# Kernel optimization log

Hardware: AMD Instinct MI355X
Metric: run time of the kernel (lower is better)

The kernel has to match this reference:

```python
import jax, jax.numpy as jnp
import numpy as np

V = 32000   # vocab_size
L = 4       # n_layer
H = 12      # n_head
C = 768     # n_embd
T = 1024    # block_size / seq len
B = 4       # batch
D = C // H  # head_dim
F = 4 * C   # mlp hidden


def setup_inputs() -> dict:
    key = jax.random.key(0)
    ks = jax.random.split(key, 12)
    n = lambda k, sh: (jax.random.normal(k, sh, dtype=jnp.float32) * 0.02)
    return {
        "idx": jax.random.randint(ks[0], (B, T), 0, V, dtype=jnp.int32),
        "tok_emb": n(ks[1], (V, C)),
        "pos_emb": n(ks[2], (T, C)),
        "Wq": n(ks[3], (L, C, C)),
        "Wk": n(ks[4], (L, C, C)),
        "Wv": n(ks[5], (L, C, C)),
        "Wp": n(ks[6], (L, C, C)),
        "bp": jnp.zeros((L, C), jnp.float32),
        "ln1s": jnp.ones((L, C), jnp.float32),
        "ln1b": jnp.zeros((L, C), jnp.float32),
        "ln2s": jnp.ones((L, C), jnp.float32),
        "ln2b": jnp.zeros((L, C), jnp.float32),
        "W1": n(ks[7], (L, C, F)),
        "b1": jnp.zeros((L, F), jnp.float32),
        "W2": n(ks[8], (L, F, C)),
        "b2": jnp.zeros((L, C), jnp.float32),
        "lnfs": jnp.ones((C,), jnp.float32),
        "lnfb": jnp.zeros((C,), jnp.float32),
        "Whead": n(ks[9], (C, V)),
    }


def _ln(x, s, b):
    m = x.mean(-1, keepdims=True)
    v = ((x - m) ** 2).mean(-1, keepdims=True)
    return (x - m) * jax.lax.rsqrt(v + 1e-5) * s + b


def reference(idx, tok_emb, pos_emb, Wq, Wk, Wv, Wp, bp, ln1s, ln1b, ln2s, ln2b,
              W1, b1, W2, b2, lnfs, lnfb, Whead):
    Bc, Tc = idx.shape
    x = tok_emb[idx] + pos_emb[None, :Tc]               # [B,T,C]
    mask = jnp.tril(jnp.ones((Tc, Tc), bool))           # causal mask
    scale = 1.0 / np.sqrt(D)
    for l in range(L):
        # --- causal self-attention (explicit QK^T, masked softmax) ---
        h = _ln(x, ln1s[l], ln1b[l])
        q = (h @ Wq[l]).reshape(Bc, Tc, H, D).transpose(0, 2, 1, 3)  # [B,H,T,D]
        k = (h @ Wk[l]).reshape(Bc, Tc, H, D).transpose(0, 2, 1, 3)
        v = (h @ Wv[l]).reshape(Bc, Tc, H, D).transpose(0, 2, 1, 3)
        att = jnp.einsum('bhqd,bhkd->bhqk', q, k) * scale            # [B,H,T,T]
        att = jnp.where(mask, att, -jnp.inf)
        att = jax.nn.softmax(att, axis=-1)
        y = jnp.einsum('bhqk,bhkd->bhqd', att, v)
        y = y.transpose(0, 2, 1, 3).reshape(Bc, Tc, C)
        x = x + (y @ Wp[l] + bp[l])
        # --- GELU MLP ---
        h = _ln(x, ln2s[l], ln2b[l])
        x = x + (jax.nn.gelu(h @ W1[l] + b1[l], approximate=False) @ W2[l] + b2[l])
    x = _ln(x, lnfs, lnfb)
    logits = x @ Whead                                  # [B,T,V]
    return logits
```

## Files before the change

kernel.cpp:

```cpp
#include <hip/hip_runtime.h>
#include <stdint.h>

#define B_ 4
#define T_ 1024
#define C_ 768
#define H_ 12
#define D_ 64
#define F_ 3072
#define V_ 32000
#define L_ 4

typedef unsigned short ushort_t;
typedef __bf16 bf16x8 __attribute__((ext_vector_type(8)));
typedef float f32x4 __attribute__((ext_vector_type(4)));
typedef unsigned short u16x8 __attribute__((ext_vector_type(8)));

__device__ __forceinline__ float b2f(unsigned short u) {
    union { unsigned int i; float f; } x; x.i = ((unsigned int)u) << 16; return x.f;
}
__device__ __forceinline__ unsigned short f2b(float f) {
    union { float f; unsigned int i; } x; x.f = f;
    unsigned int r = x.i + 0x7FFFu + ((x.i >> 16) & 1u);
    return (unsigned short)(r >> 16);
}

__device__ __forceinline__ float gelu_f(float u) {
    float z = fabsf(u) * 0.70710678118654752f;
    float t = __builtin_amdgcn_rcpf(1.0f + 0.3275911f * z);
    float poly = t * (0.254829592f + t * (-0.284496736f + t * (1.421413741f +
                 t * (-1.453152027f + t * 1.061405429f))));
    float erfz = 1.0f - poly * __expf(-z * z);
    return u * 0.5f * (1.0f + copysignf(erfz, u));
}

__device__ __forceinline__ void gload16(const ushort_t* g, ushort_t* l) {
    __builtin_amdgcn_global_load_lds(
        (const __attribute__((address_space(1))) unsigned int*)g,
        (__attribute__((address_space(3))) unsigned int*)l, 16, 0, 0);
}

__global__ __launch_bounds__(256) void k_embed(const int* __restrict__ idx,
        const float* __restrict__ tok, const float* __restrict__ pos,
        float* __restrict__ x) {
    int i = blockIdx.x * 256 + threadIdx.x;
    int m = i / (C_ / 4);
    int cc = (i % (C_ / 4)) * 4;
    int t = m & (T_ - 1);
    int tokid = idx[m];
    float4 te = *(const float4*)&tok[(size_t)tokid * C_ + cc];
    float4 pe = *(const float4*)&pos[(size_t)t * C_ + cc];
    *(float4*)&x[(size_t)m * C_ + cc] =
        make_float4(te.x + pe.x, te.y + pe.y, te.z + pe.z, te.w + pe.w);
}

__global__ __launch_bounds__(256) void k_ln(const float* __restrict__ x,
        const float* __restrict__ s, const float* __restrict__ b,
        ushort_t* __restrict__ out) {
    const int lane = threadIdx.x & 63, wave = threadIdx.x >> 6;
    const int row = blockIdx.x * 4 + wave;
    const float* xr = x + (size_t)row * C_;
    float4 v[3];
    float sum = 0.f, sq = 0.f;
#pragma unroll
    for (int j = 0; j < 3; ++j) {
        v[j] = *(const float4*)&xr[lane * 4 + j * 256];
        sum += v[j].x + v[j].y + v[j].z + v[j].w;
        sq  += v[j].x * v[j].x + v[j].y * v[j].y + v[j].z * v[j].z + v[j].w * v[j].w;
    }
#pragma unroll
    for (int off = 1; off < 64; off <<= 1) {
        sum += __shfl_xor(sum, off);
        sq  += __shfl_xor(sq,  off);
    }
    float mean = sum * (1.f / C_);
    float var  = sq * (1.f / C_) - mean * mean;
    float rstd = rsqrtf(var + 1e-5f);
#pragma unroll
    for (int j = 0; j < 3; ++j) {
        int c = lane * 4 + j * 256;
        float4 sv = *(const float4*)&s[c];
        float4 bv = *(const float4*)&b[c];
        ushort4 o;
        o.x = f2b((v[j].x - mean) * rstd * sv.x + bv.x);
        o.y = f2b((v[j].y - mean) * rstd * sv.y + bv.y);
        o.z = f2b((v[j].z - mean) * rstd * sv.z + bv.z);
        o.w = f2b((v[j].w - mean) * rstd * sv.w + bv.w);
        *(ushort4*)&out[(size_t)row * C_ + c] = o;
    }
}

__global__ void k_tcvt(const float* __restrict__ in, ushort_t* __restrict__ out,
                       int R, int C) {
    __shared__ float tile[32][33];
    const float* src = in + (size_t)blockIdx.z * R * C;
    ushort_t* dst = out + (size_t)blockIdx.z * R * C;
    int r0 = blockIdx.y * 32, c0 = blockIdx.x * 32;
    int tx = threadIdx.x, ty = threadIdx.y;
#pragma unroll
    for (int i = ty; i < 32; i += 8)
        tile[i][tx] = src[(size_t)(r0 + i) * C + c0 + tx];
    __syncthreads();
#pragma unroll
    for (int i = ty; i < 32; i += 8)
        dst[(size_t)(c0 + i) * R + r0 + tx] = f2b(tile[tx][i]);
}

__global__ void k_tcvt16(const float* __restrict__ wq, const float* __restrict__ wk,
                         const float* __restrict__ wv, const float* __restrict__ wp,
                         ushort_t* __restrict__ out) {
    __shared__ float tile[32][33];
    int l = blockIdx.z >> 2, w = blockIdx.z & 3;
    const float* src = (w == 0 ? wq : w == 1 ? wk : w == 2 ? wv : wp) + (size_t)l * C_ * C_;
    ushort_t* dst = out + (size_t)blockIdx.z * C_ * C_;
    int r0 = blockIdx.y * 32, c0 = blockIdx.x * 32;
    int tx = threadIdx.x, ty = threadIdx.y;
#pragma unroll
    for (int i = ty; i < 32; i += 8)
        tile[i][tx] = src[(size_t)(r0 + i) * C_ + c0 + tx];
    __syncthreads();
#pragma unroll
    for (int i = ty; i < 32; i += 8)
        dst[(size_t)(c0 + i) * C_ + r0 + tx] = f2b(tile[tx][i]);
}

template <int EPI>
__global__ __launch_bounds__(256) void k_gemm(
        const ushort_t* __restrict__ A, const ushort_t* __restrict__ BT,
        const float* __restrict__ bias, const float* __restrict__ resid,
        float* __restrict__ outf, ushort_t* __restrict__ outb,
        ushort_t* __restrict__ outb2, ushort_t* __restrict__ outb3,
        int M, int N, int K) {
    __shared__ __align__(16) ushort_t S[24576];
    const int tid = threadIdx.x;
    const int lane = tid & 63, wave = tid >> 6;
    const int lr = lane & 15, lg = lane >> 4;
    const int wm = (wave >> 1) * 64, wn = (wave & 1) * 64;

    const int bid = blockIdx.x;
    const int m_in = bid & 7;
    const int strip = (bid >> 3) & 3;
    const int ncol = bid >> 5;
    const int m0 = (strip * 8 + m_in) << 7;
    const int n0 = ncol << 7;

    const int sr = wave * 16 + (lane >> 2);
    const int sc = (((lane & 3) ^ ((lane >> 3) & 3)) << 3);

    f32x4 acc[4][4];
#pragma unroll
    for (int i = 0; i < 4; ++i)
#pragma unroll
        for (int j = 0; j < 4; ++j) acc[i][j] = (f32x4){0.f, 0.f, 0.f, 0.f};

    auto stage = [&](int k0, int buf) {
        ushort_t* as = S + buf * 4096;
        ushort_t* bs = S + 12288 + buf * 4096;
        gload16(&A [(size_t)(m0 + sr)      * K + k0 + sc], as + (wave * 16) * 32);
        gload16(&A [(size_t)(m0 + 64 + sr) * K + k0 + sc], as + (64 + wave * 16) * 32);
        gload16(&BT[(size_t)(n0 + sr)      * K + k0 + sc], bs + (wave * 16) * 32);
        gload16(&BT[(size_t)(n0 + 64 + sr) * K + k0 + sc], bs + (64 + wave * 16) * 32);
    };

    const int nt = K >> 5;
    stage(0, 0);
    stage(32, 1);
    int cur = 0, pre = 2;
    const int swzr = (lr >> 1) & 3;
    for (int t = 0; t < nt; ++t) {
        if (t + 1 < nt) asm volatile("s_waitcnt vmcnt(4)" ::: "memory");
        else            asm volatile("s_waitcnt vmcnt(0)" ::: "memory");
        __builtin_amdgcn_sched_barrier(0);
        __builtin_amdgcn_s_barrier();
        const ushort_t* as = S + cur * 4096;
        const ushort_t* bs = S + 12288 + cur * 4096;
        bf16x8 af[4], bfr[4];
#pragma unroll
        for (int i = 0; i < 4; ++i)
            af[i]  = *(const bf16x8*)&as[(wm + i * 16 + lr) * 32 + ((lg ^ swzr) << 3)];
#pragma unroll
        for (int j = 0; j < 4; ++j)
            bfr[j] = *(const bf16x8*)&bs[(wn + j * 16 + lr) * 32 + ((lg ^ swzr) << 3)];
        if (t + 2 < nt) stage((t + 2) << 5, pre);
#pragma unroll
        for (int i = 0; i < 4; ++i)
#pragma unroll
            for (int j = 0; j < 4; ++j)
                acc[i][j] = __builtin_amdgcn_mfma_f32_16x16x32_bf16(af[i], bfr[j], acc[i][j], 0, 0, 0);
        cur = (cur == 2) ? 0 : cur + 1;
        pre = (pre == 2) ? 0 : pre + 1;
    }

    if (EPI == 2) {
        float* cls = (float*)S;
#pragma unroll
        for (int h = 0; h < 2; ++h) {
            __syncthreads();
            if ((wm >> 6) == h) {
#pragma unroll
                for (int i = 0; i < 4; ++i)
#pragma unroll
                    for (int j = 0; j < 4; ++j)
#pragma unroll
                        for (int r = 0; r < 4; ++r)
                            cls[(i * 16 + lg * 4 + r) * 128 + wn + j * 16 + lr] = acc[i][j][r];
            }
            __syncthreads();
#pragma unroll
            for (int p = 0; p < 8; ++p) {
                int row = p * 8 + (tid >> 5);
                int colc = (tid & 31) * 4;
                f32x4 val = *(const f32x4*)&cls[row * 128 + colc];
                size_t gidx = (size_t)(m0 + h * 64 + row) * N + n0 + colc;
                f32x4 rv = *(const f32x4*)&resid[gidx];
                f32x4 bv = *(const f32x4*)&bias[n0 + colc];
                val = val + rv + bv;
                *(f32x4*)&outf[gidx] = val;
            }
        }
        return;
    }

    if (EPI == 1) {
        ushort_t* cls = S;
        __syncthreads();
#pragma unroll
        for (int i = 0; i < 4; ++i)
#pragma unroll
            for (int j = 0; j < 4; ++j) {
                float bval = bias[n0 + wn + j * 16 + lr];
#pragma unroll
                for (int r = 0; r < 4; ++r)
                    cls[(wm + i * 16 + lg * 4 + r) * 128 + wn + j * 16 + lr] =
                        f2b(gelu_f(acc[i][j][r] + bval));
            }
        __syncthreads();
#pragma unroll
        for (int p = 0; p < 8; ++p) {
            int row = p * 16 + (tid >> 4);
            int colc = (tid & 15) * 8;
            u16x8 val = *(const u16x8*)&cls[row * 128 + colc];
            *(u16x8*)&outb[(size_t)(m0 + row) * N + n0 + colc] = val;
        }
        return;
    }

#pragma unroll
    for (int i = 0; i < 4; ++i) {
#pragma unroll
        for (int j = 0; j < 4; ++j) {
            int col = n0 + wn + j * 16 + lr;
#pragma unroll
            for (int r = 0; r < 4; ++r) {
                int row = m0 + wm + i * 16 + lg * 4 + r;
                float v = acc[i][j][r];
                int nm = col / 768, c = col % 768;
                int hh = c >> 6, d = c & 63;
                int bb = row >> 10, t = row & 1023;
                ushort_t val = f2b(v);
                if (nm == 0)
                    outb [((((size_t)bb * H_ + hh) << 10) + t) * D_ + d] = val;
                else if (nm == 1)
                    outb2[((((size_t)bb * H_ + hh) << 10) + t) * D_ + d] = val;
                else
                    outb3[(((size_t)bb * H_ + hh) * D_ + d) * T_ + t] = val;
            }
        }
    }
}

__global__ __launch_bounds__(512, 2) void k_gemm256b(
        const ushort_t* __restrict__ A, const ushort_t* __restrict__ BT,
        float* __restrict__ outf, int M, int N, int K) {
    __shared__ __align__(16) ushort_t S[65536];
    const int tid = threadIdx.x;
    const int lane = tid & 63, wave = tid >> 6;
    const int lr = lane & 15, lg = lane >> 4;
    const int wm = (wave >> 2) * 128, wn = (wave & 3) * 64;

    const int bid = blockIdx.x;
    const int m_in = bid & 7;
    const int strip = (bid >> 3) & 1;
    const int ncol = bid >> 4;
    const int m0 = (strip * 8 + m_in) << 8;
    const int n0 = ncol << 8;

    const int srr = lane >> 2;
    const int sc = (((lane & 3) ^ ((lane >> 3) & 3)) << 3);

    f32x4 acc[8][4];
#pragma unroll
    for (int i = 0; i < 8; ++i)
#pragma unroll
        for (int j = 0; j < 4; ++j) acc[i][j] = (f32x4){0.f, 0.f, 0.f, 0.f};

    auto stage = [&](int k0, int buf) {
        ushort_t* as = S + buf * 8192;
        ushort_t* bs = S + 32768 + buf * 8192;
#pragma unroll
        for (int q = 0; q < 2; ++q) {
            int rb = wave * 16 + q * 128;
            gload16(&A [(size_t)(m0 + rb + srr) * K + k0 + sc], as + rb * 32);
            gload16(&BT[(size_t)(n0 + rb + srr) * K + k0 + sc], bs + rb * 32);
        }
    };

    const int nt = K >> 5;
    stage(0, 0);
    stage(32, 1);
    stage(64, 2);
    const int swzr = (lr >> 1) & 3;
    for (int t = 0; t < nt; ++t) {
        int rem = nt - 1 - t;
        if (rem >= 2)      asm volatile("s_waitcnt vmcnt(8)" ::: "memory");
        else if (rem == 1) asm volatile("s_waitcnt vmcnt(4)" ::: "memory");
        else               asm volatile("s_waitcnt vmcnt(0)" ::: "memory");
        __builtin_amdgcn_sched_barrier(0);
        __builtin_amdgcn_s_barrier();
        const ushort_t* as = S + (t & 3) * 8192;
        const ushort_t* bs = S + 32768 + (t & 3) * 8192;
        if (t + 3 < nt) stage((t + 3) << 5, (t + 3) & 3);
        bf16x8 bfr[4];
#pragma unroll
        for (int j = 0; j < 4; ++j)
            bfr[j] = *(const bf16x8*)&bs[(wn + j * 16 + lr) * 32 + ((lg ^ swzr) << 3)];
#pragma unroll
        for (int i = 0; i < 8; ++i) {
            bf16x8 af = *(const bf16x8*)&as[(wm + i * 16 + lr) * 32 + ((lg ^ swzr) << 3)];
#pragma unroll
            for (int j = 0; j < 4; ++j)
                acc[i][j] = __builtin_amdgcn_mfma_f32_16x16x32_bf16(af, bfr[j], acc[i][j], 0, 0, 0);
        }
    }

    float* cls = (float*)S;
#pragma unroll
    for (int h = 0; h < 4; ++h) {
        __syncthreads();
        if ((wm >> 7) == (h >> 1)) {
            const int ibase = (h & 1) * 4;
#pragma unroll
            for (int i2 = 0; i2 < 4; ++i2)
#pragma unroll
                for (int j = 0; j < 4; ++j)
#pragma unroll
                    for (int r = 0; r < 4; ++r)
                        cls[(i2 * 16 + lg * 4 + r) * 260 + wn + j * 16 + lr] =
                            acc[ibase + i2][j][r];
        }
        __syncthreads();
#pragma unroll
        for (int p = 0; p < 8; ++p) {
            int idx = p * 512 + tid;
            int row = idx >> 6;
            int colc = (idx & 63) * 4;
            f32x4 val = *(const f32x4*)&cls[row * 260 + colc];
            __builtin_nontemporal_store(val,
                (f32x4*)&outf[(size_t)(m0 + h * 64 + row) * N + n0 + colc]);
        }
    }
}

__global__ __launch_bounds__(256) void k_attn(const ushort_t* __restrict__ q,
        const ushort_t* __restrict__ k, const ushort_t* __restrict__ vT,
        ushort_t* __restrict__ yc) {
    __shared__ __align__(16) ushort_t P[4][16 * 136];
    const int lane = threadIdx.x & 63, wave = threadIdx.x >> 6;
    const int lr = lane & 15, lg = lane >> 4;
    const int bh = blockIdx.x;
    const int bb = bh / H_, hh = bh % H_;
    const int qrow0 = (gridDim.y - 1 - blockIdx.y) * 64 + wave * 16;
    const ushort_t* qb = q + (size_t)bh * T_ * D_;
    const ushort_t* kb = k + (size_t)bh * T_ * D_;
    const ushort_t* vb = vT + (size_t)bh * D_ * T_;

    bf16x8 aq0 = *(const bf16x8*)&qb[(qrow0 + lr) * D_ + lg * 8];
    bf16x8 aq1 = *(const bf16x8*)&qb[(qrow0 + lr) * D_ + 32 + lg * 8];

    f32x4 accY[4];
    float ls = 0.f;
#pragma unroll
    for (int d = 0; d < 4; ++d) accY[d] = (f32x4){0.f, 0.f, 0.f, 0.f};

    ushort_t* pw = &P[wave][0];
    const int kv_end = qrow0 + 16;
    for (int kv0 = 0; kv0 < kv_end; kv0 += 128) {
        const bool full = (kv0 + 127 <= qrow0);
        float p[8][4];
        float ps = 0.f;
#pragma unroll
        for (int j = 0; j < 8; ++j) {
            f32x4 s = (f32x4){0.f, 0.f, 0.f, 0.f};
            bf16x8 bk0 = *(const bf16x8*)&kb[(kv0 + j * 16 + lr) * D_ + lg * 8];
            bf16x8 bk1 = *(const bf16x8*)&kb[(kv0 + j * 16 + lr) * D_ + 32 + lg * 8];
            __builtin_amdgcn_s_setprio(1);
            s = __builtin_amdgcn_mfma_f32_16x16x32_bf16(bk0, aq0, s, 0, 0, 0);
            s = __builtin_amdgcn_mfma_f32_16x16x32_bf16(bk1, aq1, s, 0, 0, 0);
            __builtin_amdgcn_s_setprio(0);
            if (full) {
#pragma unroll
                for (int r = 0; r < 4; ++r) { p[j][r] = __expf(s[r] * 0.125f); ps += p[j][r]; }
            } else {
                int kcb = kv0 + j * 16 + lg * 4;
#pragma unroll
                for (int r = 0; r < 4; ++r) {
                    p[j][r] = (kcb + r <= qrow0 + lr) ? __expf(s[r] * 0.125f) : 0.f;
                    ps += p[j][r];
                }
            }
        }
        ps += __shfl_xor(ps, 16);
        ps += __shfl_xor(ps, 32);
        ls += ps;

        asm volatile("s_waitcnt lgkmcnt(0)" ::: "memory");
        __builtin_amdgcn_sched_barrier(0);
#pragma unroll
        for (int j = 0; j < 8; ++j) {
            unsigned int w0, w1;
            asm("v_cvt_pk_bf16_f32 %0, %1, %2" : "=v"(w0) : "v"(p[j][0]), "v"(p[j][1]));
            asm("v_cvt_pk_bf16_f32 %0, %1, %2" : "=v"(w1) : "v"(p[j][2]), "v"(p[j][3]));
            uint2 w; w.x = w0; w.y = w1;
            *(uint2*)&pw[lr * 136 + j * 16 + lg * 4] = w;
        }
        asm volatile("s_waitcnt lgkmcnt(0)" ::: "memory");
        __builtin_amdgcn_sched_barrier(0);
        bf16x8 pa[4];
#pragma unroll
        for (int ks = 0; ks < 4; ++ks)
            pa[ks] = *(const bf16x8*)&pw[lr * 136 + ks * 32 + lg * 8];
#pragma unroll
        for (int d = 0; d < 4; ++d) {
            __builtin_amdgcn_s_setprio(1);
#pragma unroll
            for (int ks = 0; ks < 4; ++ks) {
                bf16x8 bv = *(const bf16x8*)&vb[(d * 16 + lr) * T_ + kv0 + ks * 32 + lg * 8];
                accY[d] = __builtin_amdgcn_mfma_f32_16x16x32_bf16(pa[ks], bv, accY[d], 0, 0, 0);
            }
            __builtin_amdgcn_s_setprio(0);
        }
    }
    float inv[4];
#pragma unroll
    for (int r = 0; r < 4; ++r) inv[r] = 1.0f / __shfl(ls, lg * 4 + r);
#pragma unroll
    for (int d = 0; d < 4; ++d)
#pragma unroll
        for (int r = 0; r < 4; ++r) {
            int row = qrow0 + lg * 4 + r;
            yc[((size_t)bb * T_ + row) * C_ + hh * D_ + d * 16 + lr] = f2b(accY[d][r] * inv[r]);
        }
}

extern "C" void kernel_launch(void* const* d_in, const int* in_sizes, int n_in,
                              void* d_out, int out_size, void* d_ws, size_t ws_size,
                              hipStream_t stream) {
    (void)in_sizes; (void)n_in; (void)out_size; (void)ws_size;
    const int*   idx  = (const int*)d_in[0];
    const float* tok  = (const float*)d_in[1];
    const float* pos  = (const float*)d_in[2];
    const float* Wq   = (const float*)d_in[3];
    const float* Wk   = (const float*)d_in[4];
    const float* Wv   = (const float*)d_in[5];
    const float* Wp   = (const float*)d_in[6];
    const float* bp   = (const float*)d_in[7];
    const float* ln1s = (const float*)d_in[8];
    const float* ln1b = (const float*)d_in[9];
    const float* ln2s = (const float*)d_in[10];
    const float* ln2b = (const float*)d_in[11];
    const float* W1   = (const float*)d_in[12];
    const float* b1   = (const float*)d_in[13];
    const float* W2   = (const float*)d_in[14];
    const float* b2   = (const float*)d_in[15];
    const float* lnfs = (const float*)d_in[16];
    const float* lnfb = (const float*)d_in[17];
    const float* Wh   = (const float*)d_in[18];
    float* out = (float*)d_out;

    char* ws = (char*)d_ws;
    size_t off = 0;
    auto alloc = [&](size_t bytes) { void* p = ws + off; off += (bytes + 255) & ~(size_t)255; return p; };

    const size_t CCE = (size_t)C_ * C_;
    const size_t CFE = (size_t)C_ * F_;
    ushort_t* wCC  = (ushort_t*)alloc(16 * CCE * 2);
    ushort_t* w1T  = (ushort_t*)alloc((size_t)L_ * CFE * 2);
    ushort_t* w2T  = (ushort_t*)alloc((size_t)L_ * CFE * 2);
    ushort_t* whT  = (ushort_t*)alloc((size_t)C_ * V_ * 2);
    float*    x    = (float*)   alloc((size_t)B_ * T_ * C_ * 4);
    ushort_t* h    = (ushort_t*)alloc((size_t)B_ * T_ * C_ * 2);
    ushort_t* qb_  = (ushort_t*)alloc((size_t)B_ * T_ * C_ * 2);
    ushort_t* kb_  = (ushort_t*)alloc((size_t)B_ * T_ * C_ * 2);
    ushort_t* vTb  = (ushort_t*)alloc((size_t)B_ * T_ * C_ * 2);
    ushort_t* yc   = (ushort_t*)alloc((size_t)B_ * T_ * C_ * 2);
    ushort_t* mh   = (ushort_t*)alloc((size_t)B_ * T_ * F_ * 2);

    dim3 tb(32, 8);
    k_tcvt16<<<dim3(24, 24, 16), tb, 0, stream>>>(Wq, Wk, Wv, Wp, wCC);
    k_tcvt<<<dim3(96, 24, 4), tb, 0, stream>>>(W1, w1T, C_, F_);
    k_tcvt<<<dim3(24, 96, 4), tb, 0, stream>>>(W2, w2T, F_, C_);
    k_tcvt<<<dim3(1000, 24, 1), tb, 0, stream>>>(Wh, whT, C_, V_);

    k_embed<<<3072, 256, 0, stream>>>(idx, tok, pos, x);

    for (int l = 0; l < L_; ++l) {
        k_ln<<<1024, 256, 0, stream>>>(x, ln1s + l * C_, ln1b + l * C_, h);
        k_gemm<3><<<18 * 32, 256, 0, stream>>>(h, wCC + (size_t)(l * 4) * CCE,
            nullptr, nullptr, nullptr, qb_, kb_, vTb, 4096, 3 * C_, C_);
        k_attn<<<dim3(48, 16), 256, 0, stream>>>(qb_, kb_, vTb, yc);
        k_gemm<2><<<6 * 32, 256, 0, stream>>>(yc, wCC + (size_t)(l * 4 + 3) * CCE,
            bp + l * C_, x, x, nullptr, nullptr, nullptr, 4096, C_, C_);
        k_ln<<<1024, 256, 0, stream>>>(x, ln2s + l * C_, ln2b + l * C_, h);
        k_gemm<1><<<24 * 32, 256, 0, stream>>>(h, w1T + (size_t)l * CFE,
            b1 + l * F_, nullptr, nullptr, mh, nullptr, nullptr, 4096, F_, C_);
        k_gemm<2><<<6 * 32, 256, 0, stream>>>(mh, w2T + (size_t)l * CFE,
            b2 + l * C_, x, x, nullptr, nullptr, nullptr, 4096, C_, F_);
    }
    k_ln<<<1024, 256, 0, stream>>>(x, lnfs, lnfb, h);
    k_gemm256b<<<2000, 512, 0, stream>>>(h, whT, out, 4096, V_, C_);
}
```

Baseline: 1.096 ms.

## Split-K the MLP down-projection and use 128-tile GEMM for LM head

The W2 GEMM (K=3072, only 192 tiles) is split into two K-halves running as 384 blocks that write fp32 partials into the reused q buffer, followed by a reduction kernel that adds bias, residual and both partials. The LM head replaces the 256x256 512-thread kernel with the generic 128x128 kernel using a new plain-store epilogue. The goal is better CU occupancy on the under-filled GEMM. The cost is extra partial-buffer traffic and a launch, and the smaller LM-head tiles give less data reuse.

```diff
diff --git a/kernel.cpp b/kernel.cpp
--- a/kernel.cpp
+++ b/kernel.cpp
@@ -190,7 +190,7 @@
         pre = (pre == 2) ? 0 : pre + 1;
     }
 
-    if (EPI == 2) {
+    if (EPI == 0 || EPI == 2) {
         float* cls = (float*)S;
 #pragma unroll
         for (int h = 0; h < 2; ++h) {
@@ -211,10 +211,14 @@
                 int colc = (tid & 31) * 4;
                 f32x4 val = *(const f32x4*)&cls[row * 128 + colc];
                 size_t gidx = (size_t)(m0 + h * 64 + row) * N + n0 + colc;
-                f32x4 rv = *(const f32x4*)&resid[gidx];
-                f32x4 bv = *(const f32x4*)&bias[n0 + colc];
-                val = val + rv + bv;
-                *(f32x4*)&outf[gidx] = val;
+                if (EPI == 2) {
+                    f32x4 rv = *(const f32x4*)&resid[gidx];
+                    f32x4 bv = *(const f32x4*)&bias[n0 + colc];
+                    val = val + rv + bv;
+                    *(f32x4*)&outf[gidx] = val;
+                } else {
+                    __builtin_nontemporal_store(val, (f32x4*)&outf[gidx]);
+                }
             }
         }
         return;
@@ -268,96 +272,106 @@
     }
 }
 
-__global__ __launch_bounds__(512, 2) void k_gemm256b(
+__global__ __launch_bounds__(256) void k_gemm_split(
         const ushort_t* __restrict__ A, const ushort_t* __restrict__ BT,
-        float* __restrict__ outf, int M, int N, int K) {
-    __shared__ __align__(16) ushort_t S[65536];
+        float* __restrict__ part, int M, int N, int Kfull, int Klen) {
+    __shared__ __align__(16) ushort_t S[24576];
     const int tid = threadIdx.x;
     const int lane = tid & 63, wave = tid >> 6;
     const int lr = lane & 15, lg = lane >> 4;
-    const int wm = (wave >> 2) * 128, wn = (wave & 3) * 64;
+    const int wm = (wave >> 1) * 64, wn = (wave & 1) * 64;
 
     const int bid = blockIdx.x;
     const int m_in = bid & 7;
-    const int strip = (bid >> 3) & 1;
-    const int ncol = bid >> 4;
-    const int m0 = (strip * 8 + m_in) << 8;
-    const int n0 = ncol << 8;
-
-    const int srr = lane >> 2;
+    const int strip = (bid >> 3) & 3;
+    const int ncol = bid >> 5;
+    const int m0 = (strip * 8 + m_in) << 7;
+    const int n0 = ncol << 7;
+    const int kb = blockIdx.y * Klen;
+    float* outf = part + (size_t)blockIdx.y * M * N;
+
+    const int sr = wave * 16 + (lane >> 2);
     const int sc = (((lane & 3) ^ ((lane >> 3) & 3)) << 3);
 
-    f32x4 acc[8][4];
-#pragma unroll
-    for (int i = 0; i < 8; ++i)
+    f32x4 acc[4][4];
+#pragma unroll
+    for (int i = 0; i < 4; ++i)
 #pragma unroll
         for (int j = 0; j < 4; ++j) acc[i][j] = (f32x4){0.f, 0.f, 0.f, 0.f};
 
     auto stage = [&](int k0, int buf) {
-        ushort_t* as = S + buf * 8192;
-        ushort_t* bs = S + 32768 + buf * 8192;
-#pragma unroll
-        for (int q = 0; q < 2; ++q) {
-            int rb = wave * 16 + q * 128;
-            gload16(&A [(size_t)(m0 + rb + srr) * K + k0 + sc], as + rb * 32);
-            gload16(&BT[(size_t)(n0 + rb + srr) * K + k0 + sc], bs + rb * 32);
-        }
+        ushort_t* as = S + buf * 4096;
+        ushort_t* bs = S + 12288 + buf * 4096;
+        gload16(&A [(size_t)(m0 + sr)      * Kfull + kb + k0 + sc], as + (wave * 16) * 32);
+        gload16(&A [(size_t)(m0 + 64 + sr) * Kfull + kb + k0 + sc], as + (64 + wave * 16) * 32);
+        gload16(&BT[(size_t)(n0 + sr)      * Kfull + kb + k0 + sc], bs + (wave * 16) * 32);
+        gload16(&BT[(size_t)(n0 + 64 + sr) * Kfull + kb + k0 + sc], bs + (64 + wave * 16) * 32);
     };
 
-    const int nt = K >> 5;
+    const int nt = Klen >> 5;
     stage(0, 0);
     stage(32, 1);
-    stage(64, 2);
+    int cur = 0, pre = 2;
     const int swzr = (lr >> 1) & 3;
     for (int t = 0; t < nt; ++t) {
-        int rem = nt - 1 - t;
-        if (rem >= 2)      asm volatile("s_waitcnt vmcnt(8)" ::: "memory");
-        else if (rem == 1) asm volatile("s_waitcnt vmcnt(4)" ::: "memory");
-        else               asm volatile("s_waitcnt vmcnt(0)" ::: "memory");
+        if (t + 1 < nt) asm volatile("s_waitcnt vmcnt(4)" ::: "memory");
+        else            asm volatile("s_waitcnt vmcnt(0)" ::: "memory");
         __builtin_amdgcn_sched_barrier(0);
         __builtin_amdgcn_s_barrier();
-        const ushort_t* as = S + (t & 3) * 8192;
-        const ushort_t* bs = S + 32768 + (t & 3) * 8192;
-        if (t + 3 < nt) stage((t + 3) << 5, (t + 3) & 3);
-        bf16x8 bfr[4];
+        const ushort_t* as = S + cur * 4096;
+        const ushort_t* bs = S + 12288 + cur * 4096;
+        bf16x8 af[4], bfr[4];
+#pragma unroll
+        for (int i = 0; i < 4; ++i)
+            af[i]  = *(const bf16x8*)&as[(wm + i * 16 + lr) * 32 + ((lg ^ swzr) << 3)];
 #pragma unroll
         for (int j = 0; j < 4; ++j)
             bfr[j] = *(const bf16x8*)&bs[(wn + j * 16 + lr) * 32 + ((lg ^ swzr) << 3)];
-#pragma unroll
-        for (int i = 0; i < 8; ++i) {
-            bf16x8 af = *(const bf16x8*)&as[(wm + i * 16 + lr) * 32 + ((lg ^ swzr) << 3)];
+        if (t + 2 < nt) stage((t + 2) << 5, pre);
+#pragma unroll
+        for (int i = 0; i < 4; ++i)
 #pragma unroll
             for (int j = 0; j < 4; ++j)
-                acc[i][j] = __builtin_amdgcn_mfma_f32_16x16x32_bf16(af, bfr[j], acc[i][j], 0, 0, 0);
-        }
+                acc[i][j] = __builtin_amdgcn_mfma_f32_16x16x32_bf16(af[i], bfr[j], acc[i][j], 0, 0, 0);
+        cur = (cur == 2) ? 0 : cur + 1;
+        pre = (pre == 2) ? 0 : pre + 1;
     }
 
     float* cls = (float*)S;
 #pragma unroll
-    for (int h = 0; h < 4; ++h) {
+    for (int h = 0; h < 2; ++h) {
         __syncthreads();
-        if ((wm >> 7) == (h >> 1)) {
-            const int ibase = (h & 1) * 4;
-#pragma unroll
-            for (int i2 = 0; i2 < 4; ++i2)
+        if ((wm >> 6) == h) {
+#pragma unroll
+            for (int i = 0; i < 4; ++i)
 #pragma unroll
                 for (int j = 0; j < 4; ++j)
 #pragma unroll
                     for (int r = 0; r < 4; ++r)
-                        cls[(i2 * 16 + lg * 4 + r) * 260 + wn + j * 16 + lr] =
-                            acc[ibase + i2][j][r];
+                        cls[(i * 16 + lg * 4 + r) * 128 + wn + j * 16 + lr] = acc[i][j][r];
         }
         __syncthreads();
 #pragma unroll
         for (int p = 0; p < 8; ++p) {
-            int idx = p * 512 + tid;
-            int row = idx >> 6;
-            int colc = (idx & 63) * 4;
-            f32x4 val = *(const f32x4*)&cls[row * 260 + colc];
-            __builtin_nontemporal_store(val,
-                (f32x4*)&outf[(size_t)(m0 + h * 64 + row) * N + n0 + colc]);
-        }
-    }
+            int row = p * 8 + (tid >> 5);
+            int colc = (tid & 31) * 4;
+            f32x4 val = *(const f32x4*)&cls[row * 128 + colc];
+            *(f32x4*)&outf[(size_t)(m0 + h * 64 + row) * N + n0 + colc] = val;
+        }
+    }
+}
+
+__global__ __launch_bounds__(256) void k_red2(float* __restrict__ x,
+        const float* __restrict__ part, const float* __restrict__ bias) {
+    const size_t stride = (size_t)4096 * C_;
+    int i = (blockIdx.x * 256 + threadIdx.x) * 4;
+    int col = i % C_;
+    f32x4 xv = *(const f32x4*)&x[i];
+    f32x4 bv = *(const f32x4*)&bias[col];
+    f32x4 p0 = *(const f32x4*)&part[i];
+    f32x4 p1 = *(const f32x4*)&part[stride + i];
+    xv = xv + bv + p0 + p1;
+    *(f32x4*)&x[i] = xv;
 }
 
 __global__ __launch_bounds__(256) void k_attn(const ushort_t* __restrict__ q,
@@ -493,6 +507,7 @@
     ushort_t* vTb  = (ushort_t*)alloc((size_t)B_ * T_ * C_ * 2);
     ushort_t* yc   = (ushort_t*)alloc((size_t)B_ * T_ * C_ * 2);
     ushort_t* mh   = (ushort_t*)alloc((size_t)B_ * T_ * F_ * 2);
+    float* part = (float*)qb_;
 
     dim3 tb(32, 8);
     k_tcvt16<<<dim3(24, 24, 16), tb, 0, stream>>>(Wq, Wk, Wv, Wp, wCC);
@@ -512,9 +527,11 @@
         k_ln<<<1024, 256, 0, stream>>>(x, ln2s + l * C_, ln2b + l * C_, h);
         k_gemm<1><<<24 * 32, 256, 0, stream>>>(h, w1T + (size_t)l * CFE,
             b1 + l * F_, nullptr, nullptr, mh, nullptr, nullptr, 4096, F_, C_);
-        k_gemm<2><<<6 * 32, 256, 0, stream>>>(mh, w2T + (size_t)l * CFE,
-            b2 + l * C_, x, x, nullptr, nullptr, nullptr, 4096, C_, F_);
+        k_gemm_split<<<dim3(6 * 32, 2), 256, 0, stream>>>(mh, w2T + (size_t)l * CFE,
+            part, 4096, C_, F_, F_ / 2);
+        k_red2<<<3072, 256, 0, stream>>>(x, part, b2 + l * C_);
     }
     k_ln<<<1024, 256, 0, stream>>>(x, lnfs, lnfb, h);
-    k_gemm256b<<<2000, 512, 0, stream>>>(h, whT, out, 4096, V_, C_);
-}
+    k_gemm<0><<<250 * 32, 256, 0, stream>>>(h, whT, nullptr, nullptr,
+        out, nullptr, nullptr, nullptr, 4096, V_, C_);
+}
```

Result: no change. 1.104 ms (+0.7%).
